# Kernel optimization log

Measured on AMD Instinct MI355X. Metric: run time of the kernel, lower is better.

The kernel has to match this reference:

```python
import jax, jax.numpy as jnp
import numpy as np

B, S, D = 64, 4096, 256
LABELS = 50


def setup_inputs() -> dict:
    key = jax.random.key(0)
    k1, k2, k3, k4, k5, k6 = jax.random.split(key, 6)
    return {
        "find_contri": 0,
        "contri": jnp.zeros((1,), jnp.float32),  # unused on find_contri=False path
        "code_output": jax.random.normal(k1, (B, S, D), jnp.float32),
        "lengths": jax.random.randint(k2, (B,), 1, S + 1),  # valid lengths in [1, S]
        "hidden": jax.random.normal(k3, (B, D), jnp.float32),
        "W_attn": jax.random.normal(k4, (D, 2 * D), jnp.float32) * (1.0 / np.sqrt(2 * D)),
        "b_attn": jax.random.normal(k5, (D,), jnp.float32) * 0.01,
        "W_pool": jax.random.normal(k6, (LABELS, D), jnp.float32) * (1.0 / np.sqrt(D)),
    }


def reference(find_contri, contri, code_output, lengths, hidden, W_attn, b_attn, W_pool):
    b, s, d = code_output.shape
    # energy computed in the original forward but never used downstream (dead compute)
    h = jnp.broadcast_to(hidden[:, None, :], (b, s, d))
    energy = jnp.tanh(jnp.einsum('bsf,df->bsd', jnp.concatenate([h, code_output], axis=-1), W_attn) + b_attn)
    del energy
    # ragged max-pool over valid positions [0:lengths[i]) per sample (segment max)
    mask = jnp.arange(s)[None, :] < lengths[:, None]          # [B, S]
    neg_inf = jnp.asarray(-jnp.inf, code_output.dtype)
    code_pool = jnp.max(jnp.where(mask[:, :, None], code_output, neg_inf), axis=1)  # [B, D]
    attn = code_pool @ W_pool.T                                # [B, labels], no bias
    return attn
```

## Files before the change

### kernel.cpp

```cpp
#include <hip/hip_runtime.h>
#include <hip/hip_bf16.h>

#define BB  64
#define SS  4096
#define DD  256
#define LBL 50

__global__ __launch_bounds__(256) void segmax_partial_kernel(
    const float* __restrict__ code,
    const int*   __restrict__ lengths,
    float*       __restrict__ partial,
    int nchunk, int csz)
{
    int bid = blockIdx.x;
    int b   = bid / nchunk;
    int c   = bid - b * nchunk;
    int len = lengths[b];
    int s0  = c * csz;
    if (s0 >= len) return;
    int s1 = min(s0 + csz, len);

    int wave = threadIdx.x >> 6;
    int lane = threadIdx.x & 63;

    const float4* base = (const float4*)(code + (size_t)b * SS * DD);
    const float neg = -INFINITY;
    float4 m = make_float4(neg, neg, neg, neg);

    for (int s = s0 + wave; s < s1; s += 4) {
        float4 v = base[(size_t)s * (DD / 4) + lane];
        m.x = fmaxf(m.x, v.x);
        m.y = fmaxf(m.y, v.y);
        m.z = fmaxf(m.z, v.z);
        m.w = fmaxf(m.w, v.w);
    }

    __shared__ float4 red[4][64];
    red[wave][lane] = m;
    __syncthreads();

    if (threadIdx.x < 64) {
        float4 a = red[0][lane];
        #pragma unroll
        for (int w = 1; w < 4; ++w) {
            float4 v = red[w][lane];
            a.x = fmaxf(a.x, v.x);
            a.y = fmaxf(a.y, v.y);
            a.z = fmaxf(a.z, v.z);
            a.w = fmaxf(a.w, v.w);
        }
        float4* dst = (float4*)(partial + (size_t)bid * DD);
        dst[lane] = a;
    }
}

__global__ __launch_bounds__(256) void finalize_kernel(
    const float* __restrict__ partial,
    const int*   __restrict__ lengths,
    const float* __restrict__ Wp,
    float*       __restrict__ out,
    int nchunk, int csz)
{
    int b = blockIdx.x;
    int t = threadIdx.x;
    int len  = lengths[b];
    int nact = (len + csz - 1) / csz;
    if (nact > nchunk) nact = nchunk;

    float m = -INFINITY;
    const float* p = partial + (size_t)b * nchunk * DD + t;
    for (int c = 0; c < nact; ++c)
        m = fmaxf(m, p[(size_t)c * DD]);

    __shared__ float pool[DD];
    pool[t] = m;
    __syncthreads();

    if (t < LBL) {
        float acc = 0.0f;
        const float* w = Wp + (size_t)t * DD;
        #pragma unroll 8
        for (int d = 0; d < DD; ++d)
            acc += pool[d] * w[d];
        out[b * LBL + t] = acc;
    }
}

extern "C" void kernel_launch(void* const* d_in, const int* in_sizes, int n_in,
                              void* d_out, int out_size, void* d_ws, size_t ws_size,
                              hipStream_t stream) {
    const float* code    = (const float*)d_in[2];
    const int*   lengths = (const int*)  d_in[3];
    const float* Wp      = (const float*)d_in[7];
    float*       out     = (float*)d_out;
    float*       partial = (float*)d_ws;

    int nchunk = 32;
    size_t need = (size_t)BB * nchunk * DD * sizeof(float);
    while (nchunk > 1 && need > ws_size) { nchunk >>= 1; need >>= 1; }
    int csz = (SS + nchunk - 1) / nchunk;

    segmax_partial_kernel<<<BB * nchunk, 256, 0, stream>>>(code, lengths, partial, nchunk, csz);
    finalize_kernel<<<BB, 256, 0, stream>>>(partial, lengths, Wp, out, nchunk, csz);
}
```

Before: 36.09 us.

## Interleave rows across 64 chunks per sample with nontemporal loads

Result: slower. 47.57 us (+31.8%).

```diff
diff --git a/kernel.cpp b/kernel.cpp
--- a/kernel.cpp
+++ b/kernel.cpp
@@ -1,55 +1,58 @@
 #include <hip/hip_runtime.h>
-#include <hip/hip_bf16.h>
 
 #define BB  64
 #define SS  4096
 #define DD  256
 #define LBL 50
 
+#define NCHUNK 64
+#define WSLOTS (NCHUNK * 4)
+
+typedef float f4 __attribute__((ext_vector_type(4)));
+
+__device__ __forceinline__ f4 vmax4(f4 a, f4 b) {
+    f4 r;
+    r.x = fmaxf(a.x, b.x);
+    r.y = fmaxf(a.y, b.y);
+    r.z = fmaxf(a.z, b.z);
+    r.w = fmaxf(a.w, b.w);
+    return r;
+}
+
 __global__ __launch_bounds__(256) void segmax_partial_kernel(
     const float* __restrict__ code,
     const int*   __restrict__ lengths,
-    float*       __restrict__ partial,
-    int nchunk, int csz)
+    float*       __restrict__ partial)
 {
     int bid = blockIdx.x;
-    int b   = bid / nchunk;
-    int c   = bid - b * nchunk;
+    int b   = bid >> 6;
+    int c   = bid & (NCHUNK - 1);
     int len = lengths[b];
-    int s0  = c * csz;
-    if (s0 >= len) return;
-    int s1 = min(s0 + csz, len);
+    if (4 * c >= len) return;
 
     int wave = threadIdx.x >> 6;
     int lane = threadIdx.x & 63;
+    int slot = 4 * c + wave;
 
-    const float4* base = (const float4*)(code + (size_t)b * SS * DD);
+    const f4* base = (const f4*)(code + (size_t)b * SS * DD) + lane;
     const float neg = -INFINITY;
-    float4 m = make_float4(neg, neg, neg, neg);
+    f4 m = (f4){neg, neg, neg, neg};
 
-    for (int s = s0 + wave; s < s1; s += 4) {
-        float4 v = base[(size_t)s * (DD / 4) + lane];
-        m.x = fmaxf(m.x, v.x);
-        m.y = fmaxf(m.y, v.y);
-        m.z = fmaxf(m.z, v.z);
-        m.w = fmaxf(m.w, v.w);
+    for (int s = slot; s < len; s += WSLOTS) {
+        f4 v = __builtin_nontemporal_load(base + (size_t)s * (DD / 4));
+        m = vmax4(m, v);
     }
 
-    __shared__ float4 red[4][64];
+    __shared__ f4 red[4][64];
     red[wave][lane] = m;
     __syncthreads();
 
     if (threadIdx.x < 64) {
-        float4 a = red[0][lane];
+        f4 a = red[0][lane];
         #pragma unroll
-        for (int w = 1; w < 4; ++w) {
-            float4 v = red[w][lane];
-            a.x = fmaxf(a.x, v.x);
-            a.y = fmaxf(a.y, v.y);
-            a.z = fmaxf(a.z, v.z);
-            a.w = fmaxf(a.w, v.w);
-        }
-        float4* dst = (float4*)(partial + (size_t)bid * DD);
+        for (int w = 1; w < 4; ++w)
+            a = vmax4(a, red[w][lane]);
+        f4* dst = (f4*)(partial + (size_t)bid * DD);
         dst[lane] = a;
     }
 }
@@ -58,17 +61,16 @@
     const float* __restrict__ partial,
     const int*   __restrict__ lengths,
     const float* __restrict__ Wp,
-    float*       __restrict__ out,
-    int nchunk, int csz)
+    float*       __restrict__ out)
 {
     int b = blockIdx.x;
     int t = threadIdx.x;
     int len  = lengths[b];
-    int nact = (len + csz - 1) / csz;
-    if (nact > nchunk) nact = nchunk;
+    int nact = (len + 3) >> 2;
+    if (nact > NCHUNK) nact = NCHUNK;
 
     float m = -INFINITY;
-    const float* p = partial + (size_t)b * nchunk * DD + t;
+    const float* p = partial + (size_t)b * NCHUNK * DD + t;
     for (int c = 0; c < nact; ++c)
         m = fmaxf(m, p[(size_t)c * DD]);
 
@@ -95,11 +97,8 @@
     float*       out     = (float*)d_out;
     float*       partial = (float*)d_ws;
 
-    int nchunk = 32;
-    size_t need = (size_t)BB * nchunk * DD * sizeof(float);
-    while (nchunk > 1 && need > ws_size) { nchunk >>= 1; need >>= 1; }
-    int csz = (SS + nchunk - 1) / nchunk;
+    (void)ws_size;
 
-    segmax_partial_kernel<<<BB * nchunk, 256, 0, stream>>>(code, lengths, partial, nchunk, csz);
-    finalize_kernel<<<BB, 256, 0, stream>>>(partial, lengths, Wp, out, nchunk, csz);
+    segmax_partial_kernel<<<BB * NCHUNK, 256, 0, stream>>>(code, lengths, partial);
+    finalize_kernel<<<BB, 256, 0, stream>>>(partial, lengths, Wp, out);
 }
```
